# Optimization experiments

Hardware: AMD Instinct MI355X
Metric: run time of the kernel (lower is better)

## Reference

```python
import jax, jax.numpy as jnp
import numpy as np

EPS = 1e-12  # matches F.normalize clamp


def sparsemax(z):
    # Martins & Astudillo sparsemax along the last axis
    K = z.shape[-1]
    z_sorted = -jnp.sort(-z, axis=-1)                      # descending
    k = jnp.arange(1, K + 1, dtype=z.dtype)
    z_cum = jnp.cumsum(z_sorted, axis=-1)
    support = (1.0 + k * z_sorted) > z_cum                 # [..., K]
    k_z = jnp.sum(support, axis=-1, keepdims=True)         # support size
    tau = (jnp.take_along_axis(z_cum, k_z - 1, axis=-1) - 1.0) / k_z.astype(z.dtype)
    return jnp.maximum(z - tau, 0.0)


def setup_inputs() -> dict:
    key = jax.random.key(0)
    k1, k2, k3 = jax.random.split(key, 3)
    B, IN, OUT = 8192, 512, 4096
    x = jax.random.normal(k1, (B, IN), dtype=jnp.float32)
    weight = jax.random.normal(k2, (OUT, IN), dtype=jnp.float32)
    lambd = jnp.square(jax.random.normal(k3, (1,), dtype=jnp.float32))  # torch init: randn**2
    return {"x": x, "weight": weight, "lambd": lambd}


def reference(x, weight, lambd):
    # normalize prototypes and inputs onto the unit hypersphere
    w_n = weight / jnp.maximum(jnp.linalg.norm(weight, axis=-1, keepdims=True), EPS)
    x_n = x / jnp.maximum(jnp.linalg.norm(x, axis=1, keepdims=True), EPS)
    xa = x_n @ w_n.T                                        # [B, OUT]
    # ||x - a||^2 via Gram expansion (avoids [B, OUT, IN] broadcast tensor)
    x2 = jnp.sum(x_n * x_n, axis=-1, keepdims=True)         # [B, 1]
    w2 = jnp.sum(w_n * w_n, axis=-1)                        # [OUT]
    sq_dist = x2 + w2[None, :] - 2.0 * xa                   # [B, OUT]
    logits = xa - lambd * sq_dist                           # kds_mode='recon_dist'
    return sparsemax(logits)
```

## Files before the change

kernel.cpp:

```cpp
#include <hip/hip_runtime.h>

typedef __attribute__((ext_vector_type(8))) short bf16x8;
typedef __attribute__((ext_vector_type(4))) float f32x4;

__device__ inline unsigned short f2bf(float f) {
  union { float f; unsigned u; } v; v.f = f;
  unsigned r = v.u + 0x7FFFu + ((v.u >> 16) & 1u);
  return (unsigned short)(r >> 16);
}

__global__ __launch_bounds__(256) void normalize_rows_512(
    const float* __restrict__ in, unsigned short* __restrict__ out, int rows) {
  const int w = threadIdx.x >> 6, lane = threadIdx.x & 63;
  const int row = blockIdx.x * 4 + w;
  if (row >= rows) return;
  const float* p = in + (size_t)row * 512 + lane * 8;
  float4 a = *reinterpret_cast<const float4*>(p);
  float4 b = *reinterpret_cast<const float4*>(p + 4);
  float ss = a.x*a.x + a.y*a.y + a.z*a.z + a.w*a.w
           + b.x*b.x + b.y*b.y + b.z*b.z + b.w*b.w;
  #pragma unroll
  for (int off = 32; off; off >>= 1) ss += __shfl_xor(ss, off);
  const float inv = 1.0f / fmaxf(sqrtf(ss), 1e-12f);
  unsigned short o[8];
  o[0]=f2bf(a.x*inv); o[1]=f2bf(a.y*inv); o[2]=f2bf(a.z*inv); o[3]=f2bf(a.w*inv);
  o[4]=f2bf(b.x*inv); o[5]=f2bf(b.y*inv); o[6]=f2bf(b.z*inv); o[7]=f2bf(b.w*inv);
  *reinterpret_cast<uint4*>(out + (size_t)row * 512 + lane * 8) =
      *reinterpret_cast<uint4*>(o);
}

#define BM 256
#define BN 256
#define BK 32

#define STAGE_A(slot_, ko_, j_)                                                   \
  do {                                                                            \
    const int c_ = wid * 2 + (j_);                                                \
    const unsigned short* s_ = Xb + (size_t)(bm0 + c_ * 16 + srow) * 512 + (ko_) + skel; \
    __builtin_amdgcn_global_load_lds(                                             \
        (const __attribute__((address_space(1))) void*)s_,                        \
        (__attribute__((address_space(3))) void*)&As[slot_][c_ * 512], 16, 0, 0); \
  } while (0)
#define STAGE_B(slot_, ko_, j_)                                                   \
  do {                                                                            \
    const int c_ = wid * 2 + (j_);                                                \
    const unsigned short* s_ = Wb + (size_t)(bn0 + c_ * 16 + srow) * 512 + (ko_) + skel; \
    __builtin_amdgcn_global_load_lds(                                             \
        (const __attribute__((address_space(1))) void*)s_,                        \
        (__attribute__((address_space(3))) void*)&Bs[slot_][c_ * 512], 16, 0, 0); \
  } while (0)

__global__ __launch_bounds__(512, 2) void gemm_logits_f16(
    const unsigned short* __restrict__ Xb, const unsigned short* __restrict__ Wb,
    const float* __restrict__ lambd, unsigned short* __restrict__ out16) {
  __shared__ unsigned short As[3][BM * BK];
  __shared__ unsigned short Bs[3][BN * BK];
  const int tid = threadIdx.x, lane = tid & 63, wid = tid >> 6;
  const int wm = wid >> 2, wn = wid & 3;
  const int lrow = lane & 15, kg = lane >> 4;

  const int id = (int)blockIdx.x;
  const int swz = (id & 7) * 64 + (id >> 3);
  const int bx = swz & 15;
  const int by = swz >> 4;
  const int bm0 = by * BM, bn0 = bx * BN;

  const int srow = lane >> 2;
  const int skel = (lane & 3) * 8;

  f32x4 acc[8][4];
  #pragma unroll
  for (int m = 0; m < 8; ++m)
    #pragma unroll
    for (int n = 0; n < 4; ++n) { f32x4 z = {0.f,0.f,0.f,0.f}; acc[m][n] = z; }

  STAGE_A(0, 0, 0); STAGE_A(0, 0, 1); STAGE_B(0, 0, 0); STAGE_B(0, 0, 1);
  STAGE_A(1, BK, 0); STAGE_A(1, BK, 1); STAGE_B(1, BK, 0); STAGE_B(1, BK, 1);
  asm volatile("s_waitcnt vmcnt(4)" ::: "memory");
  __builtin_amdgcn_s_barrier();
  __builtin_amdgcn_sched_barrier(0);

  #pragma unroll
  for (int t = 0; t < 16; ++t) {
    const int cur = t % 3, nx2 = (t + 2) % 3;
    if (t + 2 < 16) { STAGE_A(nx2, (t + 2) * BK, 0); STAGE_A(nx2, (t + 2) * BK, 1); }
    bf16x8 af0[4], bfr[4];
    #pragma unroll
    for (int mf = 0; mf < 4; ++mf)
      af0[mf] = *reinterpret_cast<const bf16x8*>(
          &As[cur][(wm * 128 + mf * 16 + lrow) * BK + kg * 8]);
    #pragma unroll
    for (int nf = 0; nf < 4; ++nf)
      bfr[nf] = *reinterpret_cast<const bf16x8*>(
          &Bs[cur][(wn * 64 + nf * 16 + lrow) * BK + kg * 8]);
    asm volatile("s_waitcnt lgkmcnt(0)" ::: "memory");
    __builtin_amdgcn_sched_barrier(0);
    __builtin_amdgcn_s_setprio(1);
    #pragma unroll
    for (int mf = 0; mf < 4; ++mf)
      #pragma unroll
      for (int nf = 0; nf < 4; ++nf)
        acc[mf][nf] = __builtin_amdgcn_mfma_f32_16x16x32_bf16(
            af0[mf], bfr[nf], acc[mf][nf], 0, 0, 0);
    __builtin_amdgcn_s_setprio(0);
    __builtin_amdgcn_sched_barrier(0);
    if (t + 2 < 16) { STAGE_B(nx2, (t + 2) * BK, 0); STAGE_B(nx2, (t + 2) * BK, 1); }
    bf16x8 af1[4];
    #pragma unroll
    for (int mf = 0; mf < 4; ++mf)
      af1[mf] = *reinterpret_cast<const bf16x8*>(
          &As[cur][(wm * 128 + 64 + mf * 16 + lrow) * BK + kg * 8]);
    asm volatile("s_waitcnt lgkmcnt(0)" ::: "memory");
    __builtin_amdgcn_sched_barrier(0);
    __builtin_amdgcn_s_setprio(1);
    #pragma unroll
    for (int mf = 0; mf < 4; ++mf)
      #pragma unroll
      for (int nf = 0; nf < 4; ++nf)
        acc[mf + 4][nf] = __builtin_amdgcn_mfma_f32_16x16x32_bf16(
            af1[mf], bfr[nf], acc[mf + 4][nf], 0, 0, 0);
    __builtin_amdgcn_s_setprio(0);
    __builtin_amdgcn_sched_barrier(0);
    if (t < 15) {
      if (t < 13) { asm volatile("s_waitcnt vmcnt(4)" ::: "memory"); }
      else        { asm volatile("s_waitcnt vmcnt(0)" ::: "memory"); }
      __builtin_amdgcn_s_barrier();
      __builtin_amdgcn_sched_barrier(0);
    }
  }

  const float lam = lambd[0];
  const float sa_ = 1.0f + 2.0f * lam, sb_ = 2.0f * lam;
  #pragma unroll
  for (int mf = 0; mf < 8; ++mf) {
    #pragma unroll
    for (int nf = 0; nf < 4; ++nf) {
      const int gc = bn0 + wn * 64 + nf * 16 + lrow;
      #pragma unroll
      for (int r = 0; r < 4; ++r) {
        const int gr = bm0 + wm * 128 + mf * 16 + kg * 4 + r;
        union { _Float16 h; unsigned short u; } cv;
        cv.h = (_Float16)(sa_ * acc[mf][nf][r] - sb_);
        out16[(size_t)gr * 4096 + gc] = cv.u;
      }
    }
  }
}

__global__ __launch_bounds__(256) void sparsemax_f16(
    const unsigned short* __restrict__ zin, float* __restrict__ out) {
  const int tid = threadIdx.x;
  const unsigned short* zr = zin + (size_t)blockIdx.x * 4096;
  float* orow = out + (size_t)blockIdx.x * 4096;

  float v[16];
  #pragma unroll
  for (int b = 0; b < 2; ++b) {
    uint4 pk = *reinterpret_cast<const uint4*>(&zr[b * 2048 + tid * 8]);
    const unsigned short* ph = reinterpret_cast<const unsigned short*>(&pk);
    #pragma unroll
    for (int j = 0; j < 8; ++j) {
      union { unsigned short u; _Float16 h; } cv; cv.u = ph[j];
      v[b * 8 + j] = (float)cv.h;
    }
  }

  __shared__ float sred[2][4];
  __shared__ int   cred[2][4];
  const int lane = tid & 63, w = tid >> 6;

  float ls = 0.f;
  #pragma unroll
  for (int j = 0; j < 16; ++j) ls += v[j];
  #pragma unroll
  for (int off = 32; off; off >>= 1) ls += __shfl_xor(ls, off);
  if (lane == 0) sred[0][w] = ls;
  __syncthreads();
  float tau = (sred[0][0] + sred[0][1] + sred[0][2] + sred[0][3] - 1.0f)
              * (1.0f / 4096.0f);
  int prevC = 4096;

  for (int it = 0; it < 32; ++it) {
    const int pw = 1 - (it & 1);
    float s = 0.f; int c = 0;
    #pragma unroll
    for (int j = 0; j < 16; ++j) { if (v[j] > tau) { s += v[j]; ++c; } }
    #pragma unroll
    for (int off = 32; off; off >>= 1) { s += __shfl_xor(s, off); c += __shfl_xor(c, off); }
    if (lane == 0) { sred[pw][w] = s; cred[pw][w] = c; }
    __syncthreads();
    const float S = sred[pw][0] + sred[pw][1] + sred[pw][2] + sred[pw][3];
    const int   C = cred[pw][0] + cred[pw][1] + cred[pw][2] + cred[pw][3];
    tau = (S - 1.0f) / (float)C;
    if (C == prevC) break;
    prevC = C;
  }

  #pragma unroll
  for (int b = 0; b < 2; ++b) {
    float4 t0, t1;
    t0.x = fmaxf(v[b*8+0] - tau, 0.f);
    t0.y = fmaxf(v[b*8+1] - tau, 0.f);
    t0.z = fmaxf(v[b*8+2] - tau, 0.f);
    t0.w = fmaxf(v[b*8+3] - tau, 0.f);
    t1.x = fmaxf(v[b*8+4] - tau, 0.f);
    t1.y = fmaxf(v[b*8+5] - tau, 0.f);
    t1.z = fmaxf(v[b*8+6] - tau, 0.f);
    t1.w = fmaxf(v[b*8+7] - tau, 0.f);
    *reinterpret_cast<float4*>(&orow[b * 2048 + tid * 8])     = t0;
    *reinterpret_cast<float4*>(&orow[b * 2048 + tid * 8 + 4]) = t1;
  }
}

extern "C" void kernel_launch(void* const* d_in, const int* in_sizes, int n_in,
                              void* d_out, int out_size, void* d_ws, size_t ws_size,
                              hipStream_t stream) {
  const float* x     = (const float*)d_in[0];
  const float* wgt   = (const float*)d_in[1];
  const float* lambd = (const float*)d_in[2];
  float* out = (float*)d_out;

  unsigned short* xb  = (unsigned short*)d_ws;
  unsigned short* wb  = xb + (size_t)8192 * 512;
  unsigned short* z16 = wb + (size_t)4096 * 512;

  normalize_rows_512<<<8192 / 4, 256, 0, stream>>>(x, xb, 8192);
  normalize_rows_512<<<4096 / 4, 256, 0, stream>>>(wgt, wb, 4096);

  gemm_logits_f16<<<512, 512, 0, stream>>>(xb, wb, lambd, z16);

  sparsemax_f16<<<8192, 256, 0, stream>>>(z16, out);
}
```

Baseline: 113.2 us.

## Swizzle GEMM LDS layout to avoid bank conflicts and merge normalize launches

Applies an XOR swizzle on the 16-byte k-chunk position when staging A and B tiles into LDS, with the matching swizzle on fragment reads. This is meant to cut LDS bank conflicts in the MFMA operand loads. The two row-normalization launches are also merged into a single kernel covering both x and weight rows, removing one launch. The swizzle must stay consistent between the global_load_lds source offsets and the read offsets.

```diff
diff --git a/kernel.cpp b/kernel.cpp
--- a/kernel.cpp
+++ b/kernel.cpp
@@ -9,12 +9,16 @@
   return (unsigned short)(r >> 16);
 }
 
-__global__ __launch_bounds__(256) void normalize_rows_512(
-    const float* __restrict__ in, unsigned short* __restrict__ out, int rows) {
+__global__ __launch_bounds__(256) void normalize_both(
+    const float* __restrict__ x, const float* __restrict__ wgt,
+    unsigned short* __restrict__ xb, unsigned short* __restrict__ wb) {
   const int w = threadIdx.x >> 6, lane = threadIdx.x & 63;
   const int row = blockIdx.x * 4 + w;
-  if (row >= rows) return;
-  const float* p = in + (size_t)row * 512 + lane * 8;
+  const float* src;
+  unsigned short* dst;
+  if (row < 8192) { src = x + (size_t)row * 512;           dst = xb + (size_t)row * 512; }
+  else            { src = wgt + (size_t)(row - 8192) * 512; dst = wb + (size_t)(row - 8192) * 512; }
+  const float* p = src + lane * 8;
   float4 a = *reinterpret_cast<const float4*>(p);
   float4 b = *reinterpret_cast<const float4*>(p + 4);
   float ss = a.x*a.x + a.y*a.y + a.z*a.z + a.w*a.w
@@ -25,8 +29,7 @@
   unsigned short o[8];
   o[0]=f2bf(a.x*inv); o[1]=f2bf(a.y*inv); o[2]=f2bf(a.z*inv); o[3]=f2bf(a.w*inv);
   o[4]=f2bf(b.x*inv); o[5]=f2bf(b.y*inv); o[6]=f2bf(b.z*inv); o[7]=f2bf(b.w*inv);
-  *reinterpret_cast<uint4*>(out + (size_t)row * 512 + lane * 8) =
-      *reinterpret_cast<uint4*>(o);
+  *reinterpret_cast<uint4*>(dst + lane * 8) = *reinterpret_cast<uint4*>(o);
 }
 
 #define BM 256
@@ -36,7 +39,7 @@
 #define STAGE_A(slot_, ko_, j_)                                                   \
   do {                                                                            \
     const int c_ = wid * 2 + (j_);                                                \
-    const unsigned short* s_ = Xb + (size_t)(bm0 + c_ * 16 + srow) * 512 + (ko_) + skel; \
+    const unsigned short* s_ = Xb + (size_t)(bm0 + c_ * 16 + srow) * 512 + (ko_) + sskel; \
     __builtin_amdgcn_global_load_lds(                                             \
         (const __attribute__((address_space(1))) void*)s_,                        \
         (__attribute__((address_space(3))) void*)&As[slot_][c_ * 512], 16, 0, 0); \
@@ -44,7 +47,7 @@
 #define STAGE_B(slot_, ko_, j_)                                                   \
   do {                                                                            \
     const int c_ = wid * 2 + (j_);                                                \
-    const unsigned short* s_ = Wb + (size_t)(bn0 + c_ * 16 + srow) * 512 + (ko_) + skel; \
+    const unsigned short* s_ = Wb + (size_t)(bn0 + c_ * 16 + srow) * 512 + (ko_) + sskel; \
     __builtin_amdgcn_global_load_lds(                                             \
         (const __attribute__((address_space(1))) void*)s_,                        \
         (__attribute__((address_space(3))) void*)&Bs[slot_][c_ * 512], 16, 0, 0); \
@@ -65,8 +68,11 @@
   const int by = swz >> 4;
   const int bm0 = by * BM, bn0 = bx * BN;
 
-  const int srow = lane >> 2;
-  const int skel = (lane & 3) * 8;
+  const int srow  = lane >> 2;
+  const int sskel = ((lane & 3) ^ ((lane >> 3) & 3)) * 8;
+
+  const int rswz = (lrow >> 1) & 3;
+  const int kA = (kg ^ rswz) * 8;
 
   f32x4 acc[8][4];
   #pragma unroll
@@ -88,11 +94,11 @@
     #pragma unroll
     for (int mf = 0; mf < 4; ++mf)
       af0[mf] = *reinterpret_cast<const bf16x8*>(
-          &As[cur][(wm * 128 + mf * 16 + lrow) * BK + kg * 8]);
+          &As[cur][(wm * 128 + mf * 16 + lrow) * BK + kA]);
     #pragma unroll
     for (int nf = 0; nf < 4; ++nf)
       bfr[nf] = *reinterpret_cast<const bf16x8*>(
-          &Bs[cur][(wn * 64 + nf * 16 + lrow) * BK + kg * 8]);
+          &Bs[cur][(wn * 64 + nf * 16 + lrow) * BK + kA]);
     asm volatile("s_waitcnt lgkmcnt(0)" ::: "memory");
     __builtin_amdgcn_sched_barrier(0);
     __builtin_amdgcn_s_setprio(1);
@@ -109,7 +115,7 @@
     #pragma unroll
     for (int mf = 0; mf < 4; ++mf)
       af1[mf] = *reinterpret_cast<const bf16x8*>(
-          &As[cur][(wm * 128 + 64 + mf * 16 + lrow) * BK + kg * 8]);
+          &As[cur][(wm * 128 + 64 + mf * 16 + lrow) * BK + kA]);
     asm volatile("s_waitcnt lgkmcnt(0)" ::: "memory");
     __builtin_amdgcn_sched_barrier(0);
     __builtin_amdgcn_s_setprio(1);
@@ -224,8 +230,7 @@
   unsigned short* wb  = xb + (size_t)8192 * 512;
   unsigned short* z16 = wb + (size_t)4096 * 512;
 
-  normalize_rows_512<<<8192 / 4, 256, 0, stream>>>(x, xb, 8192);
-  normalize_rows_512<<<4096 / 4, 256, 0, stream>>>(wgt, wb, 4096);
+  normalize_both<<<(8192 + 4096) / 4, 256, 0, stream>>>(x, wgt, xb, wb);
 
   gemm_logits_f16<<<512, 512, 0, stream>>>(xb, wb, lambd, z16);
 
```

Result: no change. 111.7 us (-1.3%).
